# Performance work log

Hardware: AMD Instinct MI355X
Metric: run time of the kernel (lower is better)

Reference implementation:

```python
import jax, jax.numpy as jnp
import numpy as np

B, L, D, H = 2, 2048, 1024, 16
HD = D // H
SCALE = HD ** (-0.5)


def setup_inputs() -> dict:
    key = jax.random.key(0)
    ks = jax.random.split(key, 12)
    mk = lambda k, shape: (0.02 * jax.random.normal(k, shape, dtype=jnp.float32))
    return {
        "x_real": jax.random.normal(ks[0], (B, L, D), dtype=jnp.float32),
        "x_imag": jax.random.normal(ks[1], (B, L, D), dtype=jnp.float32),
        "wq_r": mk(ks[2], (D, D)),
        "wq_i": mk(ks[3], (D, D)),
        "wk_r": mk(ks[4], (D, D)),
        "wk_i": mk(ks[5], (D, D)),
        "wv_r": mk(ks[6], (D, D)),
        "wv_i": mk(ks[7], (D, D)),
        "wo_r": mk(ks[8], (D, D)),
        "wo_i": mk(ks[9], (D, D)),
        "bo_r": jnp.zeros((D,), dtype=jnp.float32),
        "bo_i": jnp.zeros((D,), dtype=jnp.float32),
    }


def _clinear(xr, xi, wr, wi):
    # (a+bi)(c+di): real = a@Wr^T - b@Wi^T ; imag = a@Wi^T + b@Wr^T
    r = xr @ wr.T - xi @ wi.T
    i = xr @ wi.T + xi @ wr.T
    return r, i


def _heads(t):
    # [B,L,D] -> [B,H,L,hd]
    return t.reshape(B, L, H, HD).transpose(0, 2, 1, 3)


def reference(x_real, x_imag, wq_r, wq_i, wk_r, wk_i, wv_r, wv_i, wo_r, wo_i, bo_r, bo_i):
    Qr, Qi = _clinear(x_real, x_imag, wq_r, wq_i)
    Kr, Ki = _clinear(x_real, x_imag, wk_r, wk_i)
    Vr, Vi = _clinear(x_real, x_imag, wv_r, wv_i)
    Qr, Qi, Kr, Ki, Vr, Vi = map(_heads, (Qr, Qi, Kr, Ki, Vr, Vi))

    # real part of complex dot product: Re(Q)Re(K)^T + Im(Q)Im(K)^T
    scores = (jnp.einsum("bhqd,bhkd->bhqk", Qr, Kr)
              + jnp.einsum("bhqd,bhkd->bhqk", Qi, Ki)) * SCALE
    causal = jnp.tril(jnp.ones((L, L), dtype=bool))
    scores = jnp.where(causal, scores, -jnp.inf)
    w = jax.nn.softmax(scores, axis=-1)

    out_r = jnp.einsum("bhqk,bhkd->bhqd", w, Vr)
    out_i = jnp.einsum("bhqk,bhkd->bhqd", w, Vi)
    merge = lambda t: t.transpose(0, 2, 1, 3).reshape(B, L, D)
    out_r, out_i = merge(out_r), merge(out_i)

    yr, yi = _clinear(out_r, out_i, wo_r, wo_i)
    return yr + bo_r, yi + bo_i
```

## Files before the change

### kernel.cpp

```cpp
#include <hip/hip_runtime.h>
#include <hip/hip_bf16.h>


using f32x4  = __attribute__((ext_vector_type(4))) float;
using short8 = __attribute__((ext_vector_type(8))) short;
using bf16_t = __hip_bfloat16;

#define AS1 __attribute__((address_space(1)))
#define AS3 __attribute__((address_space(3)))

__device__ __forceinline__ void gload_lds16(const bf16_t* g, bf16_t* l) {
  __builtin_amdgcn_global_load_lds((const AS1 unsigned int*)g, (AS3 unsigned int*)l, 16, 0, 0);
}

__device__ __forceinline__ unsigned short bfbits(float f) {
  union { bf16_t h; unsigned short u; } c; c.h = __float2bfloat16(f); return c.u;
}

__global__ void pack_x_k(const float* __restrict__ xr, const float* __restrict__ xi,
                         bf16_t* __restrict__ out) {
  const int total4 = 4096 * 2048 / 4;
  for (int idx = blockIdx.x * blockDim.x + threadIdx.x; idx < total4;
       idx += gridDim.x * blockDim.x) {
    int m = idx >> 9, k = (idx & 511) * 4;
    const float* src = (k < 1024) ? (xr + (size_t)m * 1024 + k)
                                  : (xi + (size_t)m * 1024 + (k - 1024));
    float4 v = *(const float4*)src;
    unsigned int lo = (unsigned)bfbits(v.x) | ((unsigned)bfbits(v.y) << 16);
    unsigned int hi = (unsigned)bfbits(v.z) | ((unsigned)bfbits(v.w) << 16);
    *(uint2*)(out + (size_t)idx * 4) = make_uint2(lo, hi);
  }
}

__global__ void pack_wqkv_k(const float* __restrict__ wqr, const float* __restrict__ wqi,
                            const float* __restrict__ wkr, const float* __restrict__ wki,
                            const float* __restrict__ wvr, const float* __restrict__ wvi,
                            bf16_t* __restrict__ out) {
  const int total4 = 6144 * 2048 / 4;
  for (int idx = blockIdx.x * blockDim.x + threadIdx.x; idx < total4;
       idx += gridDim.x * blockDim.x) {
    int row = idx >> 9, k = (idx & 511) * 4;
    int sec = row >> 10, r1 = row & 1023;
    bool lowk = (k < 1024);
    int kk = lowk ? k : (k - 1024);
    const float* base = wqr; float sg = 1.f;
    switch (sec) {
      case 0: base = lowk ? wqr : wqi; sg = lowk ? 1.f : -1.f; break;
      case 1: base = lowk ? wqi : wqr; break;
      case 2: base = lowk ? wkr : wki; sg = lowk ? 1.f : -1.f; break;
      case 3: base = lowk ? wki : wkr; break;
      case 4: base = lowk ? wvr : wvi; sg = lowk ? 1.f : -1.f; break;
      case 5: base = lowk ? wvi : wvr; break;
    }
    float4 v = *(const float4*)(base + (size_t)r1 * 1024 + kk);
    unsigned int lo = (unsigned)bfbits(v.x * sg) | ((unsigned)bfbits(v.y * sg) << 16);
    unsigned int hi = (unsigned)bfbits(v.z * sg) | ((unsigned)bfbits(v.w * sg) << 16);
    *(uint2*)(out + (size_t)idx * 4) = make_uint2(lo, hi);
  }
}

__global__ void pack_wo_k(const float* __restrict__ wor, const float* __restrict__ woi,
                          bf16_t* __restrict__ out) {
  const int total4 = 2048 * 2048 / 4;
  for (int idx = blockIdx.x * blockDim.x + threadIdx.x; idx < total4;
       idx += gridDim.x * blockDim.x) {
    int row = idx >> 9, k = (idx & 511) * 4;
    int sec = row >> 10, r1 = row & 1023;
    bool lowk = (k < 1024);
    int kk = lowk ? k : (k - 1024);
    const float* base; float sg = 1.f;
    if (sec == 0) { base = lowk ? wor : woi; sg = lowk ? 1.f : -1.f; }
    else          { base = lowk ? woi : wor; }
    float4 v = *(const float4*)(base + (size_t)r1 * 1024 + kk);
    unsigned int lo = (unsigned)bfbits(v.x * sg) | ((unsigned)bfbits(v.y * sg) << 16);
    unsigned int hi = (unsigned)bfbits(v.z * sg) | ((unsigned)bfbits(v.w * sg) << 16);
    *(uint2*)(out + (size_t)idx * 4) = make_uint2(lo, hi);
  }
}

__device__ __forceinline__ void gemm_core(const bf16_t* __restrict__ A,
                                          const bf16_t* __restrict__ W,
                                          int m0, int n0, f32x4 (&acc)[4][4]) {
  __shared__ __align__(16) bf16_t sA[128 * 64];
  __shared__ __align__(16) bf16_t sB[128 * 64];
  const int tid = threadIdx.x;
  const int lane = tid & 63, w = tid >> 6;
  const int wr = w >> 1, wc = w & 1;
  const int quad = lane >> 4, m16 = lane & 15;
  const int srow = w * 32 + (lane >> 3);
  const int gcol = (((lane & 7) ^ (lane >> 3)) * 8);
  const int swz7 = m16 & 7;
  for (int k0 = 0; k0 < 2048; k0 += 64) {
    __syncthreads();
#pragma unroll
    for (int i = 0; i < 4; ++i) {
      gload_lds16(A + (size_t)(m0 + srow + i * 8) * 2048 + k0 + gcol,
                  sA + (size_t)(w * 32 + i * 8) * 64 + lane * 8);
      gload_lds16(W + (size_t)(n0 + srow + i * 8) * 2048 + k0 + gcol,
                  sB + (size_t)(w * 32 + i * 8) * 64 + lane * 8);
    }
    __syncthreads();
#pragma unroll
    for (int kk = 0; kk < 2; ++kk) {
      short8 af[4], bf[4];
#pragma unroll
      for (int i = 0; i < 4; ++i)
        af[i] = *(const short8*)(sA + (wr * 64 + i * 16 + m16) * 64 +
                                 ((kk * 4 + quad) ^ swz7) * 8);
#pragma unroll
      for (int j = 0; j < 4; ++j)
        bf[j] = *(const short8*)(sB + (wc * 64 + j * 16 + m16) * 64 +
                                 ((kk * 4 + quad) ^ swz7) * 8);
#pragma unroll
      for (int i = 0; i < 4; ++i)
#pragma unroll
        for (int j = 0; j < 4; ++j)
          acc[i][j] = __builtin_amdgcn_mfma_f32_16x16x32_bf16(af[i], bf[j], acc[i][j], 0, 0, 0);
    }
  }
}

__global__ __launch_bounds__(512, 2) void gemm_qkv_k(const bf16_t* __restrict__ A,
                                                     const bf16_t* __restrict__ W,
                                                     bf16_t* __restrict__ qk,
                                                     bf16_t* __restrict__ vt) {
  __shared__ __align__(16) bf16_t sA[2][256 * 64];
  __shared__ __align__(16) bf16_t sB[2][256 * 64];
  const int tid = threadIdx.x, lane = tid & 63, w = tid >> 6;
  const int wm = w >> 2, wn = w & 3;
  const int quad = lane >> 4, m16 = lane & 15;
  const int swz7 = m16 & 7;
  const int m0 = blockIdx.x * 256, n0 = blockIdx.y * 256;
  const int NT = 32;

  const int srow = w * 16 + (lane >> 3);
  const int gcol = (((lane & 7) ^ (lane >> 3)) * 8);

  f32x4 acc[8][4] = {};

  auto stageA = [&](int buf, int half, int k0) {
#pragma unroll
    for (int i = 0; i < 2; ++i)
      gload_lds16(A + (size_t)(m0 + half * 128 + srow + i * 8) * 2048 + k0 + gcol,
                  &sA[buf][(size_t)(half * 128 + w * 16 + i * 8) * 64] + lane * 8);
  };
  auto stageB = [&](int buf, int half, int k0) {
#pragma unroll
    for (int i = 0; i < 2; ++i)
      gload_lds16(W + (size_t)(n0 + half * 128 + srow + i * 8) * 2048 + k0 + gcol,
                  &sB[buf][(size_t)(half * 128 + w * 16 + i * 8) * 64] + lane * 8);
  };

  stageA(0, 0, 0); stageA(0, 1, 0);
  stageB(0, 0, 0); stageB(0, 1, 0);
  stageA(1, 0, 64); stageA(1, 1, 64);
  asm volatile("s_waitcnt vmcnt(4)" ::: "memory");
  __builtin_amdgcn_s_barrier();

  for (int t = 0; t < NT; ++t) {
    const int p = t & 1, q = p ^ 1;
    const bf16_t* sAp = sA[p];
    const bf16_t* sBp = sB[p];
    short8 af[8][2];
#pragma unroll
    for (int nf = 0; nf < 4; ++nf) {
      if (nf == 0) {
#pragma unroll
        for (int mf = 0; mf < 8; ++mf)
#pragma unroll
          for (int kk = 0; kk < 2; ++kk)
            af[mf][kk] = *(const short8*)(sAp + (wm * 128 + mf * 16 + m16) * 64 +
                                          ((kk * 4 + quad) ^ swz7) * 8);
      }
      short8 bf[2];
#pragma unroll
      for (int kk = 0; kk < 2; ++kk)
        bf[kk] = *(const short8*)(sBp + (wn * 64 + nf * 16 + m16) * 64 +
                                  ((kk * 4 + quad) ^ swz7) * 8);
      if (nf == 0)      { if (t + 1 < NT) stageB(q, 0, (t + 1) * 64); }
      else if (nf == 1) { if (t + 1 < NT) stageB(q, 1, (t + 1) * 64); }
      else if (nf == 2) { if (t + 2 < NT) stageA(p, 0, (t + 2) * 64); }
      else              { if (t + 2 < NT) stageA(p, 1, (t + 2) * 64); }
      asm volatile("" ::: "memory");
      __builtin_amdgcn_s_barrier();
      __builtin_amdgcn_s_setprio(1);
#pragma unroll
      for (int mf = 0; mf < 8; ++mf)
#pragma unroll
        for (int kk = 0; kk < 2; ++kk)
          acc[mf][nf] = __builtin_amdgcn_mfma_f32_16x16x32_bf16(af[mf][kk], bf[kk],
                                                                acc[mf][nf], 0, 0, 0);
      __builtin_amdgcn_s_setprio(0);
      asm volatile("" ::: "memory");
      if (nf == 3) {
        if (t == NT - 2)      asm volatile("s_waitcnt vmcnt(0)" ::: "memory");
        else if (t < NT - 2)  asm volatile("s_waitcnt vmcnt(4)" ::: "memory");
      }
      __builtin_amdgcn_s_barrier();
    }
  }

#pragma unroll
  for (int mf = 0; mf < 8; ++mf) {
    const int rowb = m0 + wm * 128 + mf * 16 + quad * 4;
#pragma unroll
    for (int nf = 0; nf < 4; ++nf) {
      const int col = n0 + wn * 64 + nf * 16 + m16;
      if (col < 4096) {
        const float sc = (col < 2048) ? 0.125f : 1.f;
#pragma unroll
        for (int r = 0; r < 4; ++r)
          qk[(size_t)(rowb + r) * 4096 + col] = __float2bfloat16(acc[mf][nf][r] * sc);
      } else {
        const int vcol = col - 4096;
        const int ri = vcol >> 10, dfeat = vcol & 1023;
        const int b = rowb >> 11, seq = rowb & 2047;
        const size_t vrow = (size_t)(b * 2048 + (dfeat >> 6) * 128 + ri * 64 + (dfeat & 63));
        unsigned int lo = (unsigned)bfbits(acc[mf][nf][0]) | ((unsigned)bfbits(acc[mf][nf][1]) << 16);
        unsigned int hi = (unsigned)bfbits(acc[mf][nf][2]) | ((unsigned)bfbits(acc[mf][nf][3]) << 16);
        *(uint2*)(vt + vrow * 2048 + seq) = make_uint2(lo, hi);
      }
    }
  }
}

__global__ __launch_bounds__(256) void gemm_out_k(const bf16_t* __restrict__ A,
                                                  const bf16_t* __restrict__ W,
                                                  const float* __restrict__ bor,
                                                  const float* __restrict__ boi,
                                                  float* __restrict__ out) {
  f32x4 acc[4][4] = {};
  const int m0 = blockIdx.x * 128, n0 = blockIdx.y * 128;
  gemm_core(A, W, m0, n0, acc);
  const int lane = threadIdx.x & 63, w = threadIdx.x >> 6;
  const int wr = w >> 1, wc = w & 1, quad = lane >> 4, m16 = lane & 15;
#pragma unroll
  for (int i = 0; i < 4; ++i) {
    const int rowb = m0 + wr * 64 + i * 16 + quad * 4;
#pragma unroll
    for (int j = 0; j < 4; ++j) {
      const int col = n0 + wc * 64 + j * 16 + m16;
      float bias; float* op;
      if (col < 1024) { bias = bor[col]; op = out + col; }
      else            { bias = boi[col - 1024]; op = out + 4194304 + (col - 1024); }
#pragma unroll
      for (int r = 0; r < 4; ++r)
        op[(size_t)(rowb + r) * 1024] = acc[i][j][r] + bias;
    }
  }
}

__global__ __launch_bounds__(512, 4) void attn_k(const bf16_t* __restrict__ qk,
                                                 const bf16_t* __restrict__ vt,
                                                 bf16_t* __restrict__ acat) {
  __shared__ __align__(16) bf16_t sK[64 * 128];
  __shared__ __align__(16) bf16_t sV[144 * 64];
  __shared__ __align__(16) bf16_t sP[8][16 * 72];
  const int tid = threadIdx.x, lane = tid & 63, w = tid >> 6;
  const int wq = w & 3, sub = w >> 2;
  const int quad = lane >> 4, m16 = lane & 15;
  const int x = blockIdx.x, bh = blockIdx.y, b = bh >> 4, h = bh & 15;
  const size_t qkrow0 = (size_t)b * 2048;
  const int qA = x * 64, qB = (31 - x) * 64;
  const int nT = 32 - x;
  const int swz7 = m16 & 7;
  const int qbase = (sub ? qB : qA) + wq * 16;

  if (tid < 256) {
    const int rr = tid >> 4, cb = (tid & 15) * 4;
    const bf16_t v = __float2bfloat16(rr == 0 ? 1.f : 0.f);
#pragma unroll
    for (int i = 0; i < 4; ++i) sV[(128 + rr) * 64 + cb + i] = v;
  }

  short8 qf[4];
  {
    const bf16_t* qa = qk + (qkrow0 + qbase + m16) * 4096;
#pragma unroll
    for (int kk = 0; kk < 4; ++kk) {
      const int col = (kk >> 1) * 1024 + h * 64 + (kk & 1) * 32 + quad * 8;
      qf[kk] = *(const short8*)(qa + col);
    }
  }
  f32x4 o[9];
#pragma unroll
  for (int j = 0; j < 9; ++j) o[j] = (f32x4){0.f, 0.f, 0.f, 0.f};

  const int qrow = qbase + quad * 4;

  const int kl4 = lane >> 4, kl15 = lane & 15;
  const int vl3 = lane >> 3;
  const int vg7 = ((lane & 7) ^ vl3) * 8;

  for (int t = 0; t < nT; ++t) {
    const int k0 = t * 64;
    __syncthreads();
#pragma unroll
    for (int i = 0; i < 2; ++i) {
      const int row = w * 8 + i * 4 + kl4;
      const int g = kl15 ^ (row & 7);
      const int col = 2048 + (g >> 3) * 1024 + h * 64 + (g & 7) * 8;
      gload_lds16(qk + (qkrow0 + k0 + row) * 4096 + col,
                  sK + (size_t)(w * 8 + i * 4) * 128 + lane * 8);
    }
#pragma unroll
    for (int i = 0; i < 2; ++i) {
      const int row = w * 16 + i * 8 + vl3;
      gload_lds16(vt + ((size_t)bh * 128 + row) * 2048 + k0 + vg7,
                  sV + (size_t)(w * 16 + i * 8) * 64 + lane * 8);
    }
    __syncthreads();

    const bool act = sub ? true : (t <= x);
    if (act) {
      const bool dg = sub ? (t == nT - 1) : (t == x);

      f32x4 sv[4];
#pragma unroll
      for (int jt = 0; jt < 4; ++jt) {
        f32x4 a = (f32x4){0.f, 0.f, 0.f, 0.f};
#pragma unroll
        for (int kk = 0; kk < 4; ++kk) {
          short8 kf = *(const short8*)(sK + (jt * 16 + m16) * 128 +
                                       ((kk * 4 + quad) ^ swz7) * 8);
          a = __builtin_amdgcn_mfma_f32_16x16x32_bf16(qf[kk], kf, a, 0, 0, 0);
        }
        sv[jt] = a;
      }

      bf16_t* pw = sP[w];
#pragma unroll
      for (int jt = 0; jt < 4; ++jt)
#pragma unroll
        for (int r = 0; r < 4; ++r) {
          float s = sv[jt][r];
          if (dg && (k0 + jt * 16 + m16 > qrow + r)) s = -1e30f;
          pw[(quad * 4 + r) * 72 + jt * 16 + m16] = __float2bfloat16(__expf(s));
        }
      asm volatile("s_waitcnt lgkmcnt(0)" ::: "memory");

#pragma unroll
      for (int kc = 0; kc < 2; ++kc) {
        short8 p = *(const short8*)(pw + m16 * 72 + kc * 32 + quad * 8);
#pragma unroll
        for (int j = 0; j < 9; ++j) {
          short8 vf = *(const short8*)(sV + (j * 16 + m16) * 64 +
                                       ((kc * 4 + quad) ^ swz7) * 8);
          o[j] = __builtin_amdgcn_mfma_f32_16x16x32_bf16(p, vf, o[j], 0, 0, 0);
        }
      }
    }
  }

  float inv[4];
#pragma unroll
  for (int r = 0; r < 4; ++r)
    inv[r] = 1.f / __shfl(o[8][r], lane & 48);
#pragma unroll
  for (int j = 0; j < 8; ++j) {
    const int d = j * 16 + m16;
    const int col = (d < 64) ? (h * 64 + d) : (1024 + h * 64 + (d - 64));
#pragma unroll
    for (int r = 0; r < 4; ++r)
      acat[((size_t)b * 2048 + qrow + r) * 2048 + col] = __float2bfloat16(o[j][r] * inv[r]);
  }
}

extern "C" void kernel_launch(void* const* d_in, const int* in_sizes, int n_in,
                              void* d_out, int out_size, void* d_ws, size_t ws_size,
                              hipStream_t stream) {
  const float* xr  = (const float*)d_in[0];
  const float* xi  = (const float*)d_in[1];
  const float* wqr = (const float*)d_in[2];
  const float* wqi = (const float*)d_in[3];
  const float* wkr = (const float*)d_in[4];
  const float* wki = (const float*)d_in[5];
  const float* wvr = (const float*)d_in[6];
  const float* wvi = (const float*)d_in[7];
  const float* wor = (const float*)d_in[8];
  const float* woi = (const float*)d_in[9];
  const float* bor = (const float*)d_in[10];
  const float* boi = (const float*)d_in[11];
  float* out = (float*)d_out;

  char* ws = (char*)d_ws;
  bf16_t* Xcat = (bf16_t*)(ws);
  bf16_t* Wqkv = (bf16_t*)(ws + 16777216ull);
  bf16_t* QKb  = (bf16_t*)(ws + 41943040ull);
  bf16_t* Vt   = (bf16_t*)(ws + 75497472ull);
  bf16_t* Acat = (bf16_t*)(ws + 92274688ull);
  bf16_t* Wo   = (bf16_t*)(ws + 109051904ull);

  pack_x_k<<<2048, 256, 0, stream>>>(xr, xi, Xcat);
  pack_wqkv_k<<<2048, 256, 0, stream>>>(wqr, wqi, wkr, wki, wvr, wvi, Wqkv);
  pack_wo_k<<<1024, 256, 0, stream>>>(wor, woi, Wo);
  gemm_qkv_k<<<dim3(16, 24), 512, 0, stream>>>(Xcat, Wqkv, QKb, Vt);
  attn_k<<<dim3(16, 32), 512, 0, stream>>>(QKb, Vt, Acat);
  gemm_out_k<<<dim3(32, 16), 256, 0, stream>>>(Acat, Wo, bor, boi, out);
}
```

Baseline: 383.4 us.

## Shrink QKV GEMM N-tile to 192 and restructure MFMA phase schedule

Changes the QKV projection GEMM tile from 256x256 to 256x192, so the grid grows from 384 to 512 blocks and fills the CUs more evenly, with less accumulator register pressure. The inner loop is reorganised into four phases over k-halves and m-halves, with A prefetched one step ahead and B two steps ahead, and the vmcnt waits adjusted to match. In exchange, each block reuses loaded data less (lower arithmetic intensity) and issues more global loads.

```diff
diff --git a/kernel.cpp b/kernel.cpp
--- a/kernel.cpp
+++ b/kernel.cpp
@@ -125,76 +125,75 @@
                                                      bf16_t* __restrict__ qk,
                                                      bf16_t* __restrict__ vt) {
   __shared__ __align__(16) bf16_t sA[2][256 * 64];
-  __shared__ __align__(16) bf16_t sB[2][256 * 64];
+  __shared__ __align__(16) bf16_t sB[2][192 * 64];
   const int tid = threadIdx.x, lane = tid & 63, w = tid >> 6;
   const int wm = w >> 2, wn = w & 3;
   const int quad = lane >> 4, m16 = lane & 15;
   const int swz7 = m16 & 7;
-  const int m0 = blockIdx.x * 256, n0 = blockIdx.y * 256;
+  const int m0 = blockIdx.x * 256, n0 = blockIdx.y * 192;
   const int NT = 32;
 
-  const int srow = w * 16 + (lane >> 3);
-  const int gcol = (((lane & 7) ^ (lane >> 3)) * 8);
-
-  f32x4 acc[8][4] = {};
+  const int l3 = lane >> 3;
+  const int gcol = (((lane & 7) ^ l3) * 8);
+
+  f32x4 acc[8][3] = {};
 
   auto stageA = [&](int buf, int half, int k0) {
 #pragma unroll
     for (int i = 0; i < 2; ++i)
-      gload_lds16(A + (size_t)(m0 + half * 128 + srow + i * 8) * 2048 + k0 + gcol,
+      gload_lds16(A + (size_t)(m0 + half * 128 + w * 16 + i * 8 + l3) * 2048 + k0 + gcol,
                   &sA[buf][(size_t)(half * 128 + w * 16 + i * 8) * 64] + lane * 8);
   };
-  auto stageB = [&](int buf, int half, int k0) {
-#pragma unroll
-    for (int i = 0; i < 2; ++i)
-      gload_lds16(W + (size_t)(n0 + half * 128 + srow + i * 8) * 2048 + k0 + gcol,
-                  &sB[buf][(size_t)(half * 128 + w * 16 + i * 8) * 64] + lane * 8);
+  auto stageB = [&](int buf, int c, int k0) {
+    gload_lds16(W + (size_t)(n0 + c * 64 + w * 8 + l3) * 2048 + k0 + gcol,
+                &sB[buf][(size_t)(c * 64 + w * 8) * 64] + lane * 8);
   };
 
   stageA(0, 0, 0); stageA(0, 1, 0);
-  stageB(0, 0, 0); stageB(0, 1, 0);
-  stageA(1, 0, 64); stageA(1, 1, 64);
-  asm volatile("s_waitcnt vmcnt(4)" ::: "memory");
+  stageB(0, 0, 0); stageB(0, 1, 0); stageB(0, 2, 0);
+  stageB(1, 0, 64); stageB(1, 1, 64); stageB(1, 2, 64);
+  asm volatile("s_waitcnt vmcnt(3)" ::: "memory");
   __builtin_amdgcn_s_barrier();
 
   for (int t = 0; t < NT; ++t) {
     const int p = t & 1, q = p ^ 1;
     const bf16_t* sAp = sA[p];
     const bf16_t* sBp = sB[p];
-    short8 af[8][2];
-#pragma unroll
-    for (int nf = 0; nf < 4; ++nf) {
-      if (nf == 0) {
-#pragma unroll
-        for (int mf = 0; mf < 8; ++mf)
-#pragma unroll
-          for (int kk = 0; kk < 2; ++kk)
-            af[mf][kk] = *(const short8*)(sAp + (wm * 128 + mf * 16 + m16) * 64 +
-                                          ((kk * 4 + quad) ^ swz7) * 8);
-      }
-      short8 bf[2];
-#pragma unroll
-      for (int kk = 0; kk < 2; ++kk)
-        bf[kk] = *(const short8*)(sBp + (wn * 64 + nf * 16 + m16) * 64 +
-                                  ((kk * 4 + quad) ^ swz7) * 8);
-      if (nf == 0)      { if (t + 1 < NT) stageB(q, 0, (t + 1) * 64); }
-      else if (nf == 1) { if (t + 1 < NT) stageB(q, 1, (t + 1) * 64); }
-      else if (nf == 2) { if (t + 2 < NT) stageA(p, 0, (t + 2) * 64); }
-      else              { if (t + 2 < NT) stageA(p, 1, (t + 2) * 64); }
+    short8 af[4], bfr[3];
+#pragma unroll
+    for (int ph = 0; ph < 4; ++ph) {
+      const int kk = ph >> 1, mh = ph & 1;
+#pragma unroll
+      for (int i = 0; i < 4; ++i)
+        af[i] = *(const short8*)(sAp + (wm * 128 + (mh * 4 + i) * 16 + m16) * 64 +
+                                 ((kk * 4 + quad) ^ swz7) * 8);
+      if (mh == 0) {
+#pragma unroll
+        for (int j = 0; j < 3; ++j)
+          bfr[j] = *(const short8*)(sBp + (wn * 48 + j * 16 + m16) * 64 +
+                                    ((kk * 4 + quad) ^ swz7) * 8);
+      }
+      if (ph == 0)      { if (t + 1 < NT) stageA(q, 0, (t + 1) * 64); }
+      else if (ph == 1) { if (t + 1 < NT) stageA(q, 1, (t + 1) * 64); }
+      else if (ph == 3) {
+        if (t + 2 < NT) {
+          stageB(p, 0, (t + 2) * 64); stageB(p, 1, (t + 2) * 64); stageB(p, 2, (t + 2) * 64);
+        }
+      }
       asm volatile("" ::: "memory");
       __builtin_amdgcn_s_barrier();
       __builtin_amdgcn_s_setprio(1);
 #pragma unroll
-      for (int mf = 0; mf < 8; ++mf)
-#pragma unroll
-        for (int kk = 0; kk < 2; ++kk)
-          acc[mf][nf] = __builtin_amdgcn_mfma_f32_16x16x32_bf16(af[mf][kk], bf[kk],
-                                                                acc[mf][nf], 0, 0, 0);
+      for (int i = 0; i < 4; ++i)
+#pragma unroll
+        for (int j = 0; j < 3; ++j)
+          acc[mh * 4 + i][j] = __builtin_amdgcn_mfma_f32_16x16x32_bf16(af[i], bfr[j],
+                                                                       acc[mh * 4 + i][j], 0, 0, 0);
       __builtin_amdgcn_s_setprio(0);
       asm volatile("" ::: "memory");
-      if (nf == 3) {
+      if (ph == 3) {
         if (t == NT - 2)      asm volatile("s_waitcnt vmcnt(0)" ::: "memory");
-        else if (t < NT - 2)  asm volatile("s_waitcnt vmcnt(4)" ::: "memory");
+        else if (t < NT - 2)  asm volatile("s_waitcnt vmcnt(3)" ::: "memory");
       }
       __builtin_amdgcn_s_barrier();
     }
@@ -204,8 +203,8 @@
   for (int mf = 0; mf < 8; ++mf) {
     const int rowb = m0 + wm * 128 + mf * 16 + quad * 4;
 #pragma unroll
-    for (int nf = 0; nf < 4; ++nf) {
-      const int col = n0 + wn * 64 + nf * 16 + m16;
+    for (int nf = 0; nf < 3; ++nf) {
+      const int col = n0 + wn * 48 + nf * 16 + m16;
       if (col < 4096) {
         const float sc = (col < 2048) ? 0.125f : 1.f;
 #pragma unroll
@@ -394,7 +393,7 @@
   pack_x_k<<<2048, 256, 0, stream>>>(xr, xi, Xcat);
   pack_wqkv_k<<<2048, 256, 0, stream>>>(wqr, wqi, wkr, wki, wvr, wvi, Wqkv);
   pack_wo_k<<<1024, 256, 0, stream>>>(wor, woi, Wo);
-  gemm_qkv_k<<<dim3(16, 24), 512, 0, stream>>>(Xcat, Wqkv, QKb, Vt);
+  gemm_qkv_k<<<dim3(16, 32), 512, 0, stream>>>(Xcat, Wqkv, QKb, Vt);
   attn_k<<<dim3(16, 32), 512, 0, stream>>>(QKb, Vt, Acat);
   gemm_out_k<<<dim3(32, 16), 256, 0, stream>>>(Acat, Wo, bor, boi, out);
 }
```

Result: faster. 356.8 us (-7.0%).
